# Optimization experiments

Hardware: AMD Instinct MI355X
Metric: run time of the kernel (lower is better)

The kernel has to match this reference:

```python
import jax, jax.numpy as jnp
import numpy as np

DIM = 1024
HEADS = 16
DIM_HEAD = 64
INNER = HEADS * DIM_HEAD
LN_EPS = 1e-5


def setup_inputs() -> dict:
    key = jax.random.key(0)
    ks = jax.random.split(key, 6)
    b, n = 2, 2048
    x = jax.random.normal(ks[0], (b, n, DIM), dtype=jnp.float32)
    attn_bias = jax.random.normal(ks[1], (HEADS, n, n), dtype=jnp.float32)
    # learned params
    ln_gamma = jnp.ones((DIM,), dtype=jnp.float32)
    ln_beta = jnp.zeros((DIM,), dtype=jnp.float32)
    w_qkv = jax.random.normal(ks[2], (DIM, 3 * INNER), dtype=jnp.float32) / np.sqrt(DIM)
    w_out = jax.random.normal(ks[3], (INNER, DIM), dtype=jnp.float32) / np.sqrt(INNER)
    return {"x": x, "attn_bias": attn_bias, "ln_gamma": ln_gamma,
            "ln_beta": ln_beta, "w_qkv": w_qkv, "w_out": w_out}


def reference(x, attn_bias, ln_gamma, ln_beta, w_qkv, w_out):
    b, n, _ = x.shape
    scale = DIM_HEAD ** -0.5
    # LayerNorm
    mu = jnp.mean(x, axis=-1, keepdims=True)
    var = jnp.mean(jnp.square(x - mu), axis=-1, keepdims=True)
    xn = (x - mu) * jax.lax.rsqrt(var + LN_EPS) * ln_gamma + ln_beta
    # QKV projection: [b, n, 3*inner]
    qkv = xn @ w_qkv
    q, k, v = jnp.split(qkv, 3, axis=-1)
    # [b, n, inner] -> [b, h, n, d]
    split_heads = lambda t: t.reshape(b, n, HEADS, DIM_HEAD).transpose(0, 2, 1, 3)
    q, k, v = split_heads(q) * scale, split_heads(k), split_heads(v)
    sim = jnp.einsum('bhid,bhjd->bhij', q, k)
    sim = sim + attn_bias[None]  # broadcast over batch
    mask_value = -jnp.finfo(sim.dtype).max
    causal = jnp.triu(jnp.ones((n, n), dtype=bool), k=1)
    sim = jnp.where(causal, mask_value, sim)
    attn = jax.nn.softmax(sim, axis=-1)
    out = jnp.einsum('bhij,bhjd->bhid', attn, v)
    out = out.transpose(0, 2, 1, 3).reshape(b, n, INNER)
    return out @ w_out
```

## Files before the change

kernel.cpp:

```cpp
#include <hip/hip_runtime.h>
#include <hip/hip_bf16.h>
#include <math.h>

typedef unsigned short u16;
typedef __attribute__((ext_vector_type(8))) __bf16 bf16x8;
typedef __attribute__((ext_vector_type(4))) float f32x4;

static __device__ __forceinline__ u16 f2bf(float f) {
    unsigned int u = __builtin_bit_cast(unsigned int, f);
    u += 0x7fffu + ((u >> 16) & 1u);
    return (u16)(u >> 16);
}

__global__ __launch_bounds__(256) void prep_kernel(
    const float* __restrict__ x, const float* __restrict__ g,
    const float* __restrict__ bta, u16* __restrict__ xn,
    const float* __restrict__ wqkv, u16* __restrict__ wqkvT,
    const float* __restrict__ wout, u16* __restrict__ woutT)
{
    const int bid = blockIdx.x;
    const int tid = threadIdx.x;
    if (bid < 4096) {
        const int row = bid;
        const float4 v = *(const float4*)&x[(size_t)row * 1024 + tid * 4];
        float s  = v.x + v.y + v.z + v.w;
        float s2 = v.x * v.x + v.y * v.y + v.z * v.z + v.w * v.w;
        #pragma unroll
        for (int off = 32; off; off >>= 1) {
            s  += __shfl_xor(s,  off);
            s2 += __shfl_xor(s2, off);
        }
        __shared__ float red[8];
        if ((tid & 63) == 0) { red[tid >> 6] = s; red[4 + (tid >> 6)] = s2; }
        __syncthreads();
        s  = red[0] + red[1] + red[2] + red[3];
        s2 = red[4] + red[5] + red[6] + red[7];
        const float mean = s * (1.0f / 1024.0f);
        const float var  = s2 * (1.0f / 1024.0f) - mean * mean;
        const float rstd = rsqrtf(var + 1e-5f);
        const float4 gg = *(const float4*)&g[tid * 4];
        const float4 bb = *(const float4*)&bta[tid * 4];
        ushort4 o;
        o.x = f2bf((v.x - mean) * rstd * gg.x + bb.x);
        o.y = f2bf((v.y - mean) * rstd * gg.y + bb.y);
        o.z = f2bf((v.z - mean) * rstd * gg.z + bb.z);
        o.w = f2bf((v.w - mean) * rstd * gg.w + bb.w);
        *(ushort4*)&xn[(size_t)row * 1024 + tid * 4] = o;
    } else {
        const float* in; u16* outT; int N, idx;
        if (bid < 4864) { in = wqkv; outT = wqkvT; N = 3072; idx = bid - 4096; }
        else            { in = wout; outT = woutT; N = 1024; idx = bid - 4864; }
        const int K = 1024;
        const int k0 = (idx & 15) * 64, n0 = (idx >> 4) * 64;
        __shared__ u16 tile[64][72];
        #pragma unroll
        for (int i = 0; i < 4; ++i) {
            int c = tid + i * 256;
            int kr = c >> 4, nc = (c & 15) * 4;
            float4 v = *(const float4*)&in[(size_t)(k0 + kr) * N + n0 + nc];
            tile[nc + 0][kr] = f2bf(v.x);
            tile[nc + 1][kr] = f2bf(v.y);
            tile[nc + 2][kr] = f2bf(v.z);
            tile[nc + 3][kr] = f2bf(v.w);
        }
        __syncthreads();
        #pragma unroll
        for (int i = 0; i < 4; ++i) {
            int c = tid + i * 256;
            int nr = c >> 4, kc = (c & 15) * 4;
            ushort4 w = *(const ushort4*)&tile[nr][kc];
            *(ushort4*)&outT[(size_t)(n0 + nr) * K + k0 + kc] = w;
        }
    }
}

template <int EPI, int BN>
__global__ __launch_bounds__(256) void gemm_bf16_k(
    const u16* __restrict__ A, const u16* __restrict__ Bt,
    int M, int N, int K,
    float* __restrict__ Cf,
    u16* __restrict__ Qo, u16* __restrict__ Ko, u16* __restrict__ Vo)
{
    constexpr int NF = BN / 32;
    __shared__ u16 lds[2][4096 + BN * 32];
    const int tid = threadIdx.x;
    const int lane = tid & 63, w = tid >> 6;
    const int l15 = lane & 15, l4 = lane >> 4;
    const int wm = w & 1, wn = w >> 1;

    const int nwg = gridDim.x * gridDim.y;
    int lin = blockIdx.y * gridDim.x + blockIdx.x;
    lin = (lin & 7) * (nwg >> 3) + (lin >> 3);
    const int bx = lin % gridDim.x, by = lin / gridDim.x;
    const int n0 = bx * BN, m0 = by * 128;

    auto stage = [&](int buf, int kt) {
        const u16* Ab = A + (size_t)m0 * K + kt * 32;
        const u16* Bb = Bt + (size_t)n0 * K + kt * 32;
        #pragma unroll
        for (int i = 0; i < 2; ++i) {
            int c = tid + (i << 8);
            int r = c >> 2, ke = (c & 3) * 8;
            __builtin_amdgcn_global_load_lds(
                (const __attribute__((address_space(1))) void*)(Ab + (size_t)r * K + ke),
                (__attribute__((address_space(3))) void*)(&lds[buf][0] + c * 8), 16, 0, 0);
        }
        #pragma unroll
        for (int i = 0; i < BN / 64; ++i) {
            int c = tid + (i << 8);
            int r = c >> 2, ke = (c & 3) * 8;
            __builtin_amdgcn_global_load_lds(
                (const __attribute__((address_space(1))) void*)(Bb + (size_t)r * K + ke),
                (__attribute__((address_space(3))) void*)(&lds[buf][4096] + c * 8), 16, 0, 0);
        }
    };

    f32x4 acc[4][NF];
    #pragma unroll
    for (int mf = 0; mf < 4; ++mf)
        #pragma unroll
        for (int nf = 0; nf < NF; ++nf)
            acc[mf][nf] = f32x4{0.f, 0.f, 0.f, 0.f};

    const int NT = K >> 5;
    stage(0, 0);
    __syncthreads();
    for (int kt = 0; kt < NT; ++kt) {
        const int buf = kt & 1;
        if (kt + 1 < NT) stage(buf ^ 1, kt + 1);
        const u16* Ab = &lds[buf][0];
        const u16* Bb = &lds[buf][4096];
        bf16x8 af[4], bfv[NF];
        #pragma unroll
        for (int mf = 0; mf < 4; ++mf)
            af[mf] = *(const bf16x8*)(Ab + (wm * 64 + mf * 16 + l15) * 32 + l4 * 8);
        #pragma unroll
        for (int nf = 0; nf < NF; ++nf)
            bfv[nf] = *(const bf16x8*)(Bb + (wn * (BN / 2) + nf * 16 + l15) * 32 + l4 * 8);
        #pragma unroll
        for (int mf = 0; mf < 4; ++mf)
            #pragma unroll
            for (int nf = 0; nf < NF; ++nf)
                acc[mf][nf] = __builtin_amdgcn_mfma_f32_16x16x32_bf16(
                    af[mf], bfv[nf], acc[mf][nf], 0, 0, 0);
        __syncthreads();
    }

    #pragma unroll
    for (int mf = 0; mf < 4; ++mf) {
        #pragma unroll
        for (int nf = 0; nf < NF; ++nf) {
            #pragma unroll
            for (int r = 0; r < 4; ++r) {
                const int row = m0 + wm * 64 + mf * 16 + l4 * 4 + r;
                const int col = n0 + wn * (BN / 2) + nf * 16 + l15;
                const float v = acc[mf][nf][r];
                if (EPI == 1) {
                    Cf[(size_t)row * N + col] = v;
                } else {
                    const int t = col >> 10, rem = col & 1023;
                    const int h = rem >> 6, d = rem & 63;
                    const int b = row >> 11, nn = row & 2047;
                    const size_t idx = ((size_t)((b * 16 + h) * 2048 + nn)) * 64 + d;
                    if (t == 0)      Qo[idx] = f2bf(v * 0.125f);
                    else if (t == 1) Ko[idx] = f2bf(v);
                    else             Vo[idx] = f2bf(v);
                }
            }
        }
    }
}

__global__ __launch_bounds__(512, 2) void attn_kernel(
    const u16* __restrict__ Q, const u16* __restrict__ Kmat,
    const u16* __restrict__ Vmat, const float* __restrict__ bias,
    u16* __restrict__ att)
{
    const int hb = blockIdx.x;
    const int h = hb >> 1, b = hb & 1;
    const int bh = b * 16 + h;
    const int y = blockIdx.y;
    const int qb = (y < 8) ? y : 23 - y;
    const int q0 = qb << 7;
    const int tid = threadIdx.x;
    const int w = tid >> 6, lane = tid & 63;
    const int l15 = lane & 15, l4 = lane >> 4;

    __shared__ u16 K_lds[2][64][72];
    __shared__ u16 V_lds[2][64][66];
    __shared__ u16 P_lds[8][16][72];

    const int qrow_a = q0 + w * 16 + l15;
    bf16x8 qa[2];
    #pragma unroll
    for (int ks = 0; ks < 2; ++ks)
        qa[ks] = *(const bf16x8*)(Q + ((size_t)bh * 2048 + qrow_a) * 64 + ks * 32 + l4 * 8);

    f32x4 acc_o[4];
    #pragma unroll
    for (int nf = 0; nf < 4; ++nf) acc_o[nf] = f32x4{0.f, 0.f, 0.f, 0.f};
    float m_r[4], l_r[4];
    #pragma unroll
    for (int r = 0; r < 4; ++r) { m_r[r] = -INFINITY; l_r[r] = 0.f; }

    const int qrow_c = q0 + w * 16 + l4 * 4;
    const int qlim = q0 + w * 16 + 15;
    const float* biasrow = bias + (size_t)h * 2048 * 2048;

    const int rr_s = tid >> 3, pp_s = (tid & 7) * 8;
    int4 kreg, vreg;
    auto issue_loads = [&](int j0n) {
        kreg = *(const int4*)&Kmat[((size_t)bh * 2048 + j0n + rr_s) * 64 + pp_s];
        vreg = *(const int4*)&Vmat[((size_t)bh * 2048 + j0n + rr_s) * 64 + pp_s];
    };
    auto load_bias = [&](int j0n, float (&dst)[4][4]) {
        #pragma unroll
        for (int nf = 0; nf < 4; ++nf)
            #pragma unroll
            for (int r = 0; r < 4; ++r)
                dst[nf][r] = biasrow[(size_t)(qrow_c + r) * 2048 + j0n + nf * 16 + l15];
    };

    const int NT = 2 * qb + 2;
    float bregA[4][4], bregB[4][4];

    issue_loads(0);
    load_bias(0, bregA);

    auto tile_step = [&](int jt, float (&bcur)[4][4], float (&bnext)[4][4]) {
        const int j0 = jt << 6;
        const int buf = jt & 1;
        *(int4*)&K_lds[buf][rr_s][pp_s] = kreg;
        {
            union { int4 v; u16 u[8]; } uu; uu.v = vreg;
            #pragma unroll
            for (int j = 0; j < 8; ++j)
                V_lds[buf][pp_s + j][rr_s] = uu.u[j];
        }
        if (jt + 1 < NT) {
            issue_loads((jt + 1) << 6);
            if (((jt + 1) << 6) <= qlim) load_bias((jt + 1) << 6, bnext);
        }
        __builtin_amdgcn_sched_barrier(0);
        asm volatile("s_waitcnt lgkmcnt(0)" ::: "memory");
        __builtin_amdgcn_s_barrier();
        __builtin_amdgcn_sched_barrier(0);

        if (j0 <= qlim) {
            f32x4 s[4];
            #pragma unroll
            for (int nf = 0; nf < 4; ++nf) s[nf] = f32x4{0.f, 0.f, 0.f, 0.f};
            __builtin_amdgcn_s_setprio(1);
            #pragma unroll
            for (int ks = 0; ks < 2; ++ks)
                #pragma unroll
                for (int nf = 0; nf < 4; ++nf) {
                    bf16x8 kb = *(const bf16x8*)&K_lds[buf][nf * 16 + l15][ks * 32 + l4 * 8];
                    s[nf] = __builtin_amdgcn_mfma_f32_16x16x32_bf16(qa[ks], kb, s[nf], 0, 0, 0);
                }
            __builtin_amdgcn_s_setprio(0);

            float p[4][4];
            if (j0 + 63 > q0 + w * 16) {
                #pragma unroll
                for (int nf = 0; nf < 4; ++nf) {
                    const int col = j0 + nf * 16 + l15;
                    #pragma unroll
                    for (int r = 0; r < 4; ++r) {
                        const int qr = qrow_c + r;
                        float v = s[nf][r] + bcur[nf][r];
                        p[nf][r] = (col > qr) ? -1e30f : v;
                    }
                }
            } else {
                #pragma unroll
                for (int nf = 0; nf < 4; ++nf)
                    #pragma unroll
                    for (int r = 0; r < 4; ++r)
                        p[nf][r] = s[nf][r] + bcur[nf][r];
            }

            float mt[4];
            #pragma unroll
            for (int r = 0; r < 4; ++r)
                mt[r] = fmaxf(fmaxf(p[0][r], p[1][r]), fmaxf(p[2][r], p[3][r]));
            int need = 0;
            #pragma unroll
            for (int r = 0; r < 4; ++r) need |= (mt[r] > m_r[r] + 8.0f);
            if (__any(need)) {
                #pragma unroll
                for (int off = 1; off < 16; off <<= 1)
                    #pragma unroll
                    for (int r = 0; r < 4; ++r) mt[r] = fmaxf(mt[r], __shfl_xor(mt[r], off));
                #pragma unroll
                for (int r = 0; r < 4; ++r) {
                    const float mn = fmaxf(m_r[r], mt[r]);
                    const float alpha = __expf(m_r[r] - mn);
                    m_r[r] = mn;
                    l_r[r] *= alpha;
                    #pragma unroll
                    for (int nf = 0; nf < 4; ++nf) acc_o[nf][r] *= alpha;
                }
            }

            float ps[4] = {0.f, 0.f, 0.f, 0.f};
            #pragma unroll
            for (int nf = 0; nf < 4; ++nf)
                #pragma unroll
                for (int r = 0; r < 4; ++r) {
                    const float e = __expf(p[nf][r] - m_r[r]);
                    ps[r] += e;
                    P_lds[w][l4 * 4 + r][nf * 16 + l15] = f2bf(e);
                }
            #pragma unroll
            for (int off = 1; off < 16; off <<= 1)
                #pragma unroll
                for (int r = 0; r < 4; ++r) ps[r] += __shfl_xor(ps[r], off);
            #pragma unroll
            for (int r = 0; r < 4; ++r) l_r[r] += ps[r];

            __builtin_amdgcn_s_setprio(1);
            #pragma unroll
            for (int ks = 0; ks < 2; ++ks) {
                bf16x8 pa = *(const bf16x8*)&P_lds[w][l15][ks * 32 + l4 * 8];
                #pragma unroll
                for (int nf = 0; nf < 4; ++nf) {
                    bf16x8 vb = *(const bf16x8*)&V_lds[buf][nf * 16 + l15][ks * 32 + l4 * 8];
                    acc_o[nf] = __builtin_amdgcn_mfma_f32_16x16x32_bf16(pa, vb, acc_o[nf], 0, 0, 0);
                }
            }
            __builtin_amdgcn_s_setprio(0);
        }
    };

    for (int jt = 0; jt < NT; jt += 2) {
        tile_step(jt,     bregA, bregB);
        tile_step(jt + 1, bregB, bregA);
    }

    #pragma unroll
    for (int nf = 0; nf < 4; ++nf)
        #pragma unroll
        for (int r = 0; r < 4; ++r) {
            const int qr = qrow_c + r;
            const float o = acc_o[nf][r] / l_r[r];
            att[((size_t)b * 2048 + qr) * 1024 + h * 64 + nf * 16 + l15] = f2bf(o);
        }
}

extern "C" void kernel_launch(void* const* d_in, const int* in_sizes, int n_in,
                              void* d_out, int out_size, void* d_ws, size_t ws_size,
                              hipStream_t stream) {
    const float* x     = (const float*)d_in[0];
    const float* bias  = (const float*)d_in[1];
    const float* gamma = (const float*)d_in[2];
    const float* beta_ = (const float*)d_in[3];
    const float* wqkv  = (const float*)d_in[4];
    const float* wout  = (const float*)d_in[5];
    float* out = (float*)d_out;

    char* ws = (char*)d_ws;
    u16* xn     = (u16*)(ws + 0);
    u16* wqkvT  = (u16*)(ws + 8388608);
    u16* woutT  = (u16*)(ws + 14680064);
    u16* Qb     = (u16*)(ws + 16777216);
    u16* Kb     = (u16*)(ws + 25165824);
    u16* Vb     = (u16*)(ws + 33554432);
    u16* attb   = xn;

    prep_kernel<<<5120, 256, 0, stream>>>(x, gamma, beta_, xn, wqkv, wqkvT, wout, woutT);
    gemm_bf16_k<0, 128><<<dim3(24, 32), 256, 0, stream>>>(xn, wqkvT, 4096, 3072, 1024,
                                                          nullptr, Qb, Kb, Vb);
    attn_kernel<<<dim3(32, 16), 512, 0, stream>>>(Qb, Kb, Vb, bias, attb);
    gemm_bf16_k<1, 64><<<dim3(16, 32), 256, 0, stream>>>(attb, woutT, 4096, 1024, 1024,
                                                         out, nullptr, nullptr, nullptr);
}
```

Measured before the change: 142.7 us.

## Store V transposed from QKV GEMM epilogue to drop LDS transpose in attention

The QKV GEMM epilogue now writes V in a [b,h,d,n] transposed layout using 4-element vector stores. The attention kernel can then load V rows with one 16-byte LDS store instead of eight scattered 2-byte transposed writes. The V LDS tile is padded to 72 columns to match K, and the block-to-head mapping changes from interleaved to contiguous. In exchange, the GEMM epilogue writes to V with a 4 KB stride between neighbouring lanes, which may coalesce poorly.

After: 131.9 us, median of 2. -7.5%, faster.

```diff
diff --git a/kernel.cpp b/kernel.cpp
--- a/kernel.cpp
+++ b/kernel.cpp
@@ -79,7 +79,7 @@
     const u16* __restrict__ A, const u16* __restrict__ Bt,
     int M, int N, int K,
     float* __restrict__ Cf,
-    u16* __restrict__ Qo, u16* __restrict__ Ko, u16* __restrict__ Vo)
+    u16* __restrict__ Qo, u16* __restrict__ Ko, u16* __restrict__ Vto)
 {
     constexpr int NF = BN / 32;
     __shared__ u16 lds[2][4096 + BN * 32];
@@ -150,21 +150,28 @@
     for (int mf = 0; mf < 4; ++mf) {
         #pragma unroll
         for (int nf = 0; nf < NF; ++nf) {
-            #pragma unroll
-            for (int r = 0; r < 4; ++r) {
-                const int row = m0 + wm * 64 + mf * 16 + l4 * 4 + r;
-                const int col = n0 + wn * (BN / 2) + nf * 16 + l15;
-                const float v = acc[mf][nf][r];
-                if (EPI == 1) {
-                    Cf[(size_t)row * N + col] = v;
+            const int row0 = m0 + wm * 64 + mf * 16 + l4 * 4;
+            const int col  = n0 + wn * (BN / 2) + nf * 16 + l15;
+            if (EPI == 1) {
+                #pragma unroll
+                for (int r = 0; r < 4; ++r)
+                    Cf[(size_t)(row0 + r) * N + col] = acc[mf][nf][r];
+            } else {
+                const int t = col >> 10, rem = col & 1023;
+                const int h = rem >> 6, d = rem & 63;
+                const int b0 = row0 >> 11, nn0 = row0 & 2047;
+                if (t == 2) {
+                    union { ushort4 v; u16 e[4]; } vv;
+                    #pragma unroll
+                    for (int r = 0; r < 4; ++r) vv.e[r] = f2bf(acc[mf][nf][r]);
+                    *(ushort4*)&Vto[((size_t)((b0 * 16 + h) * 64) + d) * 2048 + nn0] = vv.v;
                 } else {
-                    const int t = col >> 10, rem = col & 1023;
-                    const int h = rem >> 6, d = rem & 63;
-                    const int b = row >> 11, nn = row & 2047;
-                    const size_t idx = ((size_t)((b * 16 + h) * 2048 + nn)) * 64 + d;
-                    if (t == 0)      Qo[idx] = f2bf(v * 0.125f);
-                    else if (t == 1) Ko[idx] = f2bf(v);
-                    else             Vo[idx] = f2bf(v);
+                    #pragma unroll
+                    for (int r = 0; r < 4; ++r) {
+                        const size_t idx = ((size_t)((b0 * 16 + h) * 2048 + nn0 + r)) * 64 + d;
+                        if (t == 0) Qo[idx] = f2bf(acc[mf][nf][r] * 0.125f);
+                        else        Ko[idx] = f2bf(acc[mf][nf][r]);
+                    }
                 }
             }
         }
@@ -173,11 +180,11 @@
 
 __global__ __launch_bounds__(512, 2) void attn_kernel(
     const u16* __restrict__ Q, const u16* __restrict__ Kmat,
-    const u16* __restrict__ Vmat, const float* __restrict__ bias,
+    const u16* __restrict__ Vt, const float* __restrict__ bias,
     u16* __restrict__ att)
 {
     const int hb = blockIdx.x;
-    const int h = hb >> 1, b = hb & 1;
+    const int h = hb & 15, b = hb >> 4;
     const int bh = b * 16 + h;
     const int y = blockIdx.y;
     const int qb = (y < 8) ? y : 23 - y;
@@ -187,7 +194,7 @@
     const int l15 = lane & 15, l4 = lane >> 4;
 
     __shared__ u16 K_lds[2][64][72];
-    __shared__ u16 V_lds[2][64][66];
+    __shared__ u16 V_lds[2][64][72];
     __shared__ u16 P_lds[8][16][72];
 
     const int qrow_a = q0 + w * 16 + l15;
@@ -211,7 +218,7 @@
     int4 kreg, vreg;
     auto issue_loads = [&](int j0n) {
         kreg = *(const int4*)&Kmat[((size_t)bh * 2048 + j0n + rr_s) * 64 + pp_s];
-        vreg = *(const int4*)&Vmat[((size_t)bh * 2048 + j0n + rr_s) * 64 + pp_s];
+        vreg = *(const int4*)&Vt[((size_t)bh * 64 + rr_s) * 2048 + j0n + pp_s];
     };
     auto load_bias = [&](int j0n, float (&dst)[4][4]) {
         #pragma unroll
@@ -231,12 +238,7 @@
         const int j0 = jt << 6;
         const int buf = jt & 1;
         *(int4*)&K_lds[buf][rr_s][pp_s] = kreg;
-        {
-            union { int4 v; u16 u[8]; } uu; uu.v = vreg;
-            #pragma unroll
-            for (int j = 0; j < 8; ++j)
-                V_lds[buf][pp_s + j][rr_s] = uu.u[j];
-        }
+        *(int4*)&V_lds[buf][rr_s][pp_s] = vreg;
         if (jt + 1 < NT) {
             issue_loads((jt + 1) << 6);
             if (((jt + 1) << 6) <= qlim) load_bias((jt + 1) << 6, bnext);
@@ -365,13 +367,13 @@
     u16* woutT  = (u16*)(ws + 14680064);
     u16* Qb     = (u16*)(ws + 16777216);
     u16* Kb     = (u16*)(ws + 25165824);
-    u16* Vb     = (u16*)(ws + 33554432);
+    u16* Vtb    = (u16*)(ws + 33554432);
     u16* attb   = xn;
 
     prep_kernel<<<5120, 256, 0, stream>>>(x, gamma, beta_, xn, wqkv, wqkvT, wout, woutT);
     gemm_bf16_k<0, 128><<<dim3(24, 32), 256, 0, stream>>>(xn, wqkvT, 4096, 3072, 1024,
-                                                          nullptr, Qb, Kb, Vb);
-    attn_kernel<<<dim3(32, 16), 512, 0, stream>>>(Qb, Kb, Vb, bias, attb);
+                                                          nullptr, Qb, Kb, Vtb);
+    attn_kernel<<<dim3(32, 16), 512, 0, stream>>>(Qb, Kb, Vtb, bias, attb);
     gemm_bf16_k<1, 64><<<dim3(16, 32), 256, 0, stream>>>(attb, woutT, 4096, 1024, 1024,
                                                          out, nullptr, nullptr, nullptr);
 }
```
